# Kernel optimization log

Hardware: AMD Instinct MI355X
Metric: run time of the kernel (lower is better)

The kernel has to match this reference:

```python
import jax, jax.numpy as jnp
import numpy as np

N = 50000      # nodes
E = 800000     # edges (avg degree 16)
D_IN = 128
H = 128
D_OUT = 64
L = 3          # num GCNConv layers


def setup_inputs() -> dict:
    key = jax.random.key(0)
    ks = jax.random.split(key, 9)
    x = jax.random.normal(ks[0], (N, D_IN), jnp.float32)
    edge_index = jax.random.randint(ks[1], (2, E), 0, N, dtype=jnp.int32)
    s_in = 1.0 / np.sqrt(D_IN)
    s_h = 1.0 / np.sqrt(H)
    W1 = jax.random.normal(ks[2], (D_IN, H), jnp.float32) * s_in
    b1 = jnp.zeros((H,), jnp.float32)
    Wc = jax.random.normal(ks[3], (L, H, H), jnp.float32) * s_h
    bc = jnp.zeros((L, H), jnp.float32)
    W2 = jax.random.normal(ks[4], (H, D_OUT), jnp.float32) * s_h
    b2 = jnp.zeros((D_OUT,), jnp.float32)
    return {"x": x, "edge_index": edge_index, "W1": W1, "b1": b1,
            "Wc": Wc, "bc": bc, "W2": W2, "b2": b2}


def reference(x, edge_index, W1, b1, Wc, bc, W2, b2):
    n = x.shape[0]
    src, dst = edge_index[0], edge_index[1]
    # GCNConv normalization with self-loops: deg[i] = 1 + in-degree(i)
    deg = jnp.zeros((n,), x.dtype).at[dst].add(1.0) + 1.0
    dis = jax.lax.rsqrt(deg)                       # D^{-1/2}
    norm = dis[src] * dis[dst]                     # per-edge norm, [E]
    self_norm = (dis * dis)[:, None]               # self-loop norm, [n,1]
    # dnn1: Linear + ReLU
    h = jax.nn.relu(x @ W1 + b1)
    # GCNConv layers: x' = D^{-1/2}(A+I)D^{-1/2} X W + b
    for l in range(Wc.shape[0]):
        hw = h @ Wc[l]                             # [n, H]
        msg = hw[src] * norm[:, None]              # gather + scale, [E, H]
        agg = jax.ops.segment_sum(msg, dst, num_segments=n)
        h = agg + self_norm * hw + bc[l]
    # dnn2: Linear
    return h @ W2 + b2
```

## Files before the change

### kernel.cpp

```cpp
#include <hip/hip_runtime.h>
#include <hip/hip_fp16.h>


typedef _Float16 f16;
typedef __attribute__((ext_vector_type(8))) _Float16 f16x8;
typedef __attribute__((ext_vector_type(4))) float f32x4;

constexpr int H = 128;
constexpr int CH = 512;


__global__ __launch_bounds__(256) void k_degree(const int* __restrict__ dst,
                                                int* __restrict__ cnt,
                                                int* __restrict__ rank, int E) {
    int e = blockIdx.x * 256 + threadIdx.x;
    if (e < E) rank[e] = atomicAdd(&cnt[dst[e]], 1);
}

__global__ __launch_bounds__(CH) void k_scan1(const int* __restrict__ cnt,
                                              int* __restrict__ roff,
                                              int* __restrict__ csum,
                                              float* __restrict__ dis,
                                              float* __restrict__ dis2, int n) {
    __shared__ int sh[CH];
    int t = threadIdx.x;
    int i = blockIdx.x * CH + t;
    int v = (i < n) ? cnt[i] : 0;
    if (i < n) {
        float r = rsqrtf((float)(v + 1));
        dis[i] = r;
        dis2[i] = r * r;
    }
    sh[t] = v;
    __syncthreads();
    for (int off = 1; off < CH; off <<= 1) {
        int x = (t >= off) ? sh[t - off] : 0;
        __syncthreads();
        sh[t] += x;
        __syncthreads();
    }
    if (i < n) roff[i] = sh[t] - v;
    if (t == CH - 1) csum[blockIdx.x] = sh[t];
}

__global__ __launch_bounds__(256) void k_scan2(const int* __restrict__ csum,
                                               int* __restrict__ coff, int nch) {
    __shared__ int sh[256];
    int t = threadIdx.x;
    int v = (t < nch) ? csum[t] : 0;
    sh[t] = v;
    __syncthreads();
    for (int off = 1; off < 256; off <<= 1) {
        int x = (t >= off) ? sh[t - off] : 0;
        __syncthreads();
        sh[t] += x;
        __syncthreads();
    }
    if (t < nch) coff[t] = sh[t] - v;
}

__global__ __launch_bounds__(256) void k_scan3(int* __restrict__ roff,
                                               const int* __restrict__ coff,
                                               int n, int E) {
    int i = blockIdx.x * 256 + threadIdx.x;
    if (i < n) roff[i] += coff[i / CH];
    if (i == 0) roff[n] = E;
}

__global__ __launch_bounds__(256) void k_fill(const int* __restrict__ src,
                                              const int* __restrict__ dst,
                                              const int* __restrict__ rank,
                                              const int* __restrict__ roff,
                                              const float* __restrict__ dis,
                                              unsigned long long* __restrict__ edata,
                                              int E) {
    int e = blockIdx.x * 256 + threadIdx.x;
    if (e < E) {
        int d = dst[e], s = src[e];
        int pos = roff[d] + rank[e];
        float nm = dis[s] * dis[d];
        unsigned long long v = (unsigned long long)(unsigned)s |
                               ((unsigned long long)__float_as_uint(nm) << 32);
        atomicExch(&edata[pos], v);
    }
}


__global__ __launch_bounds__(256) void k_cvt_w(const float* __restrict__ W1,
                                               const float* __restrict__ Wc,
                                               const float* __restrict__ W2,
                                               f16* __restrict__ BT1,
                                               f16* __restrict__ BTc,
                                               f16* __restrict__ BT2) {
    int i = blockIdx.x * 256 + threadIdx.x;
    if (i < 16384) {
        int c = i >> 7, k = i & 127;
        BT1[i] = (f16)W1[k * 128 + c];
    } else if (i < 65536) {
        int j = i - 16384;
        int l = j >> 14, r = j & 16383;
        int c = r >> 7, k = r & 127;
        BTc[j] = (f16)Wc[l * 16384 + k * 128 + c];
    } else if (i < 73728) {
        int j = i - 65536;
        int c = j >> 7, k = j & 127;
        BT2[j] = (f16)W2[k * 64 + c];
    }
}


template <int NCOLS, int MODE, bool AF32>
__global__ __launch_bounds__(256) void k_gemm16(const void* __restrict__ Av,
                                                const f16* __restrict__ BT,
                                                const float* __restrict__ bias,
                                                void* __restrict__ Cv, int n) {
    constexpr int CT = NCOLS / 16;
    constexpr int BSTR = H + 8;
    __shared__ f16 Bs[NCOLS * BSTR];

    const int tid = threadIdx.x;
    constexpr int CHUNKS = NCOLS * H / (256 * 8);
#pragma unroll
    for (int it = 0; it < CHUNKS; ++it) {
        int idx = tid + it * 256;
        int r = idx >> 4;
        int c8 = idx & 15;
        *(f16x8*)&Bs[r * BSTR + c8 * 8] = *(const f16x8*)&BT[r * H + c8 * 8];
    }
    __syncthreads();

    const int l = tid & 63;
    const int w = tid >> 6;
    const int lrow = l & 15;
    const int lk = (l >> 4) * 8;
    int arow = blockIdx.x * 64 + w * 16 + lrow;
    int arc = arow < n ? arow : n - 1;

    f16x8 a[4];
    if constexpr (AF32) {
        const float* ap = (const float*)Av + (size_t)arc * H;
#pragma unroll
        for (int ks = 0; ks < 4; ++ks) {
            float4 u = *(const float4*)&ap[ks * 32 + lk];
            float4 v = *(const float4*)&ap[ks * 32 + lk + 4];
            f16x8 t;
            t[0] = (f16)u.x; t[1] = (f16)u.y; t[2] = (f16)u.z; t[3] = (f16)u.w;
            t[4] = (f16)v.x; t[5] = (f16)v.y; t[6] = (f16)v.z; t[7] = (f16)v.w;
            a[ks] = t;
        }
    } else {
        const f16* ap = (const f16*)Av + (size_t)arc * H;
#pragma unroll
        for (int ks = 0; ks < 4; ++ks) a[ks] = *(const f16x8*)&ap[ks * 32 + lk];
    }

    f32x4 acc[CT];
#pragma unroll
    for (int ct = 0; ct < CT; ++ct) acc[ct] = (f32x4)(0.f);

#pragma unroll
    for (int ks = 0; ks < 4; ++ks) {
#pragma unroll
        for (int ct = 0; ct < CT; ++ct) {
            f16x8 b = *(const f16x8*)&Bs[(ct * 16 + lrow) * BSTR + ks * 32 + lk];
            acc[ct] = __builtin_amdgcn_mfma_f32_16x16x32_f16(a[ks], b, acc[ct], 0, 0, 0);
        }
    }

    const int rbase = blockIdx.x * 64 + w * 16 + (l >> 4) * 4;
#pragma unroll
    for (int ct = 0; ct < CT; ++ct) {
        int col = ct * 16 + lrow;
        float bv = 0.f;
        if constexpr (MODE != 0) bv = bias[col];
#pragma unroll
        for (int r = 0; r < 4; ++r) {
            int row = rbase + r;
            if (row >= n) continue;
            float v = acc[ct][r] + bv;
            if constexpr (MODE == 1) v = fmaxf(v, 0.f);
            if constexpr (MODE == 2)
                ((float*)Cv)[(size_t)row * NCOLS + col] = v;
            else
                ((f16*)Cv)[(size_t)row * NCOLS + col] = (f16)v;
        }
    }
}


__global__ __launch_bounds__(256) void k_agg16(const __half2* __restrict__ hw,
                                               const int* __restrict__ roff,
                                               const long long* __restrict__ edata,
                                               const float* __restrict__ dis2,
                                               const float* __restrict__ bias,
                                               unsigned int* __restrict__ hout, int n) {
    int wave = threadIdx.x >> 6;
    int lane = threadIdx.x & 63;
    int node = blockIdx.x * 4 + wave;
    if (node >= n) return;

    int e0 = roff[node];
    int e1 = roff[node + 1];

    float2 sv = __half22float2(hw[(size_t)node * 64 + lane]);
    float d2 = dis2[node];
    float ax = sv.x * d2, ay = sv.y * d2;

    int e = e0;
    for (; e + 8 <= e1; e += 8) {
        long long ed[8];
#pragma unroll
        for (int j = 0; j < 8; ++j) ed[j] = __builtin_nontemporal_load(&edata[e + j]);
        float2 v[8];
#pragma unroll
        for (int j = 0; j < 8; ++j)
            v[j] = __half22float2(hw[(size_t)(unsigned)(ed[j] & 0xffffffff) * 64 + lane]);
#pragma unroll
        for (int j = 0; j < 8; ++j) {
            float nm = __int_as_float((int)(ed[j] >> 32));
            ax = fmaf(nm, v[j].x, ax);
            ay = fmaf(nm, v[j].y, ay);
        }
    }
    for (; e + 2 <= e1; e += 2) {
        long long d0 = __builtin_nontemporal_load(&edata[e]);
        long long d1 = __builtin_nontemporal_load(&edata[e + 1]);
        float2 v0 = __half22float2(hw[(size_t)(unsigned)(d0 & 0xffffffff) * 64 + lane]);
        float2 v1 = __half22float2(hw[(size_t)(unsigned)(d1 & 0xffffffff) * 64 + lane]);
        ax = fmaf(__int_as_float((int)(d0 >> 32)), v0.x, ax);
        ay = fmaf(__int_as_float((int)(d0 >> 32)), v0.y, ay);
        ax = fmaf(__int_as_float((int)(d1 >> 32)), v1.x, ax);
        ay = fmaf(__int_as_float((int)(d1 >> 32)), v1.y, ay);
    }
    for (; e < e1; ++e) {
        long long d0 = __builtin_nontemporal_load(&edata[e]);
        float2 v0 = __half22float2(hw[(size_t)(unsigned)(d0 & 0xffffffff) * 64 + lane]);
        float nm = __int_as_float((int)(d0 >> 32));
        ax = fmaf(nm, v0.x, ax);
        ay = fmaf(nm, v0.y, ay);
    }

    float2 b = ((const float2*)bias)[lane];
    ax += b.x; ay += b.y;
    __half2 r = __float22half2_rn(make_float2(ax, ay));
    __builtin_nontemporal_store(*(unsigned int*)&r, &hout[(size_t)node * 64 + lane]);
}


extern "C" void kernel_launch(void* const* d_in, const int* in_sizes, int n_in,
                              void* d_out, int out_size, void* d_ws, size_t ws_size,
                              hipStream_t stream) {
    const float* x  = (const float*)d_in[0];
    const int*   ei = (const int*)d_in[1];
    const float* W1 = (const float*)d_in[2];
    const float* b1 = (const float*)d_in[3];
    const float* Wc = (const float*)d_in[4];
    const float* bc = (const float*)d_in[5];
    const float* W2 = (const float*)d_in[6];
    const float* b2 = (const float*)d_in[7];
    float* out = (float*)d_out;

    const int n = in_sizes[0] / H;
    const int E = in_sizes[1] / 2;
    const int* src = ei;
    const int* dst = ei + E;

    char* p = (char*)d_ws;
    auto alloc = [&](size_t b) -> void* {
        void* r = (void*)p;
        p += (b + 255) & ~(size_t)255;
        return r;
    };
    f16*   h    = (f16*)alloc((size_t)n * H * 2);
    f16*   hw   = (f16*)alloc((size_t)n * H * 2);
    f16*   BT1  = (f16*)alloc(16384 * 2);
    f16*   BTc  = (f16*)alloc(3 * 16384 * 2);
    f16*   BT2  = (f16*)alloc(8192 * 2);
    int*   cnt  = (int*)alloc((size_t)n * 4);
    int*   rank = (int*)alloc((size_t)E * 4);
    int*   roff = (int*)alloc((size_t)(n + 1) * 4);
    const int nch = (n + CH - 1) / CH;
    int*   csum = (int*)alloc((size_t)nch * 4);
    int*   coff = (int*)alloc((size_t)nch * 4);
    unsigned long long* edata = (unsigned long long*)alloc((size_t)E * 8);
    float* dis  = (float*)alloc((size_t)n * 4);
    float* dis2 = (float*)alloc((size_t)n * 4);

    hipMemsetAsync(cnt, 0, (size_t)n * 4, stream);

    k_degree<<<(E + 255) / 256, 256, 0, stream>>>(dst, cnt, rank, E);
    k_scan1<<<nch, CH, 0, stream>>>(cnt, roff, csum, dis, dis2, n);
    k_scan2<<<1, 256, 0, stream>>>(csum, coff, nch);
    k_scan3<<<(n + 255) / 256, 256, 0, stream>>>(roff, coff, n, E);
    k_fill<<<(E + 255) / 256, 256, 0, stream>>>(src, dst, rank, roff, dis, edata, E);

    k_cvt_w<<<288, 256, 0, stream>>>(W1, Wc, W2, BT1, BTc, BT2);

    const int gblk = (n + 63) / 64;
    k_gemm16<128, 1, true><<<gblk, 256, 0, stream>>>(x, BT1, b1, h, n);
    for (int l = 0; l < 3; ++l) {
        k_gemm16<128, 0, false><<<gblk, 256, 0, stream>>>(h, BTc + (size_t)l * 16384, nullptr, hw, n);
        k_agg16<<<(n + 3) / 4, 256, 0, stream>>>((const __half2*)hw, roff, (const long long*)edata,
                                                 dis2, bc + (size_t)l * H, (unsigned int*)h, n);
    }
    k_gemm16<64, 2, false><<<gblk, 256, 0, stream>>>(h, BT2, b2, out, n);
}
```

Before: 337.6 us.

## Pad CSR rows to multiples of eight and software-pipeline edge loads in aggregation

The CSR layout now pads each node's edge list to a multiple of 8 and zero-fills the padding, so the aggregation kernel can run a single unrolled 8-wide loop with no remainder loops. Each iteration prefetches the next 8 edge records before gathering the current ones. The kernel also moves to 512-thread blocks with normal rather than nontemporal loads and stores, and the weight conversion is merged into the degree kernel to save a launch. In exchange it adds a memset of the enlarged edge buffer and wasted gathers on padded zero-weight entries, which all read node 0.

```diff
diff --git a/kernel.cpp b/kernel.cpp
--- a/kernel.cpp
+++ b/kernel.cpp
@@ -10,11 +10,34 @@
 constexpr int CH = 512;
 
 
-__global__ __launch_bounds__(256) void k_degree(const int* __restrict__ dst,
-                                                int* __restrict__ cnt,
-                                                int* __restrict__ rank, int E) {
-    int e = blockIdx.x * 256 + threadIdx.x;
-    if (e < E) rank[e] = atomicAdd(&cnt[dst[e]], 1);
+__global__ __launch_bounds__(256) void k_degree_cvtw(const int* __restrict__ dst,
+                                                     int* __restrict__ cnt,
+                                                     int* __restrict__ rank, int E, int EB,
+                                                     const float* __restrict__ W1,
+                                                     const float* __restrict__ Wc,
+                                                     const float* __restrict__ W2,
+                                                     f16* __restrict__ BT1,
+                                                     f16* __restrict__ BTc,
+                                                     f16* __restrict__ BT2) {
+    if (blockIdx.x < (unsigned)EB) {
+        int e = blockIdx.x * 256 + threadIdx.x;
+        if (e < E) rank[e] = atomicAdd(&cnt[dst[e]], 1);
+    } else {
+        int i = (blockIdx.x - EB) * 256 + threadIdx.x;
+        if (i < 16384) {
+            int c = i >> 7, k = i & 127;
+            BT1[i] = (f16)W1[k * 128 + c];
+        } else if (i < 65536) {
+            int j = i - 16384;
+            int l = j >> 14, r = j & 16383;
+            int c = r >> 7, k = r & 127;
+            BTc[j] = (f16)Wc[l * 16384 + k * 128 + c];
+        } else if (i < 73728) {
+            int j = i - 65536;
+            int c = j >> 7, k = j & 127;
+            BT2[j] = (f16)W2[k * 64 + c];
+        }
+    }
 }
 
 __global__ __launch_bounds__(CH) void k_scan1(const int* __restrict__ cnt,
@@ -31,7 +54,8 @@
         dis[i] = r;
         dis2[i] = r * r;
     }
-    sh[t] = v;
+    int pd = (v + 7) & ~7;
+    sh[t] = pd;
     __syncthreads();
     for (int off = 1; off < CH; off <<= 1) {
         int x = (t >= off) ? sh[t - off] : 0;
@@ -39,12 +63,13 @@
         sh[t] += x;
         __syncthreads();
     }
-    if (i < n) roff[i] = sh[t] - v;
+    if (i < n) roff[i] = sh[t] - pd;
     if (t == CH - 1) csum[blockIdx.x] = sh[t];
 }
 
 __global__ __launch_bounds__(256) void k_scan2(const int* __restrict__ csum,
-                                               int* __restrict__ coff, int nch) {
+                                               int* __restrict__ coff,
+                                               int* __restrict__ roff, int n, int nch) {
     __shared__ int sh[256];
     int t = threadIdx.x;
     int v = (t < nch) ? csum[t] : 0;
@@ -57,14 +82,13 @@
         __syncthreads();
     }
     if (t < nch) coff[t] = sh[t] - v;
+    if (t == nch - 1) roff[n] = sh[t];
 }
 
 __global__ __launch_bounds__(256) void k_scan3(int* __restrict__ roff,
-                                               const int* __restrict__ coff,
-                                               int n, int E) {
+                                               const int* __restrict__ coff, int n) {
     int i = blockIdx.x * 256 + threadIdx.x;
     if (i < n) roff[i] += coff[i / CH];
-    if (i == 0) roff[n] = E;
 }
 
 __global__ __launch_bounds__(256) void k_fill(const int* __restrict__ src,
@@ -86,29 +110,6 @@
 }
 
 
-__global__ __launch_bounds__(256) void k_cvt_w(const float* __restrict__ W1,
-                                               const float* __restrict__ Wc,
-                                               const float* __restrict__ W2,
-                                               f16* __restrict__ BT1,
-                                               f16* __restrict__ BTc,
-                                               f16* __restrict__ BT2) {
-    int i = blockIdx.x * 256 + threadIdx.x;
-    if (i < 16384) {
-        int c = i >> 7, k = i & 127;
-        BT1[i] = (f16)W1[k * 128 + c];
-    } else if (i < 65536) {
-        int j = i - 16384;
-        int l = j >> 14, r = j & 16383;
-        int c = r >> 7, k = r & 127;
-        BTc[j] = (f16)Wc[l * 16384 + k * 128 + c];
-    } else if (i < 73728) {
-        int j = i - 65536;
-        int c = j >> 7, k = j & 127;
-        BT2[j] = (f16)W2[k * 64 + c];
-    }
-}
-
-
 template <int NCOLS, int MODE, bool AF32>
 __global__ __launch_bounds__(256) void k_gemm16(const void* __restrict__ Av,
                                                 const f16* __restrict__ BT,
@@ -188,7 +189,7 @@
 }
 
 
-__global__ __launch_bounds__(256) void k_agg16(const __half2* __restrict__ hw,
+__global__ __launch_bounds__(512) void k_agg16(const __half2* __restrict__ hw,
                                                const int* __restrict__ roff,
                                                const long long* __restrict__ edata,
                                                const float* __restrict__ dis2,
@@ -196,54 +197,46 @@
                                                unsigned int* __restrict__ hout, int n) {
     int wave = threadIdx.x >> 6;
     int lane = threadIdx.x & 63;
-    int node = blockIdx.x * 4 + wave;
+    int node = blockIdx.x * 8 + wave;
     if (node >= n) return;
 
-    int e0 = roff[node];
-    int e1 = roff[node + 1];
+    int e = roff[node];
+    const int e1 = roff[node + 1];
 
     float2 sv = __half22float2(hw[(size_t)node * 64 + lane]);
     float d2 = dis2[node];
     float ax = sv.x * d2, ay = sv.y * d2;
 
-    int e = e0;
-    for (; e + 8 <= e1; e += 8) {
-        long long ed[8];
-#pragma unroll
-        for (int j = 0; j < 8; ++j) ed[j] = __builtin_nontemporal_load(&edata[e + j]);
+    long long cur[8], nxt[8];
+    if (e < e1) {
+#pragma unroll
+        for (int j = 0; j < 8; ++j) cur[j] = edata[e + j];
+    }
+    while (e < e1) {
+        int en = e + 8;
+        if (en < e1) {
+#pragma unroll
+            for (int j = 0; j < 8; ++j) nxt[j] = edata[en + j];
+        }
         float2 v[8];
 #pragma unroll
         for (int j = 0; j < 8; ++j)
-            v[j] = __half22float2(hw[(size_t)(unsigned)(ed[j] & 0xffffffff) * 64 + lane]);
+            v[j] = __half22float2(hw[(size_t)(unsigned)(cur[j] & 0xffffffff) * 64 + lane]);
 #pragma unroll
         for (int j = 0; j < 8; ++j) {
-            float nm = __int_as_float((int)(ed[j] >> 32));
+            float nm = __int_as_float((int)(cur[j] >> 32));
             ax = fmaf(nm, v[j].x, ax);
             ay = fmaf(nm, v[j].y, ay);
         }
-    }
-    for (; e + 2 <= e1; e += 2) {
-        long long d0 = __builtin_nontemporal_load(&edata[e]);
-        long long d1 = __builtin_nontemporal_load(&edata[e + 1]);
-        float2 v0 = __half22float2(hw[(size_t)(unsigned)(d0 & 0xffffffff) * 64 + lane]);
-        float2 v1 = __half22float2(hw[(size_t)(unsigned)(d1 & 0xffffffff) * 64 + lane]);
-        ax = fmaf(__int_as_float((int)(d0 >> 32)), v0.x, ax);
-        ay = fmaf(__int_as_float((int)(d0 >> 32)), v0.y, ay);
-        ax = fmaf(__int_as_float((int)(d1 >> 32)), v1.x, ax);
-        ay = fmaf(__int_as_float((int)(d1 >> 32)), v1.y, ay);
-    }
-    for (; e < e1; ++e) {
-        long long d0 = __builtin_nontemporal_load(&edata[e]);
-        float2 v0 = __half22float2(hw[(size_t)(unsigned)(d0 & 0xffffffff) * 64 + lane]);
-        float nm = __int_as_float((int)(d0 >> 32));
-        ax = fmaf(nm, v0.x, ax);
-        ay = fmaf(nm, v0.y, ay);
+#pragma unroll
+        for (int j = 0; j < 8; ++j) cur[j] = nxt[j];
+        e = en;
     }
 
     float2 b = ((const float2*)bias)[lane];
     ax += b.x; ay += b.y;
     __half2 r = __float22half2_rn(make_float2(ax, ay));
-    __builtin_nontemporal_store(*(unsigned int*)&r, &hout[(size_t)node * 64 + lane]);
+    hout[(size_t)node * 64 + lane] = *(unsigned int*)&r;
 }
 
 
@@ -282,25 +275,27 @@
     const int nch = (n + CH - 1) / CH;
     int*   csum = (int*)alloc((size_t)nch * 4);
     int*   coff = (int*)alloc((size_t)nch * 4);
-    unsigned long long* edata = (unsigned long long*)alloc((size_t)E * 8);
+    const size_t ecap = (size_t)E + 8 * (size_t)n;
+    unsigned long long* edata = (unsigned long long*)alloc(ecap * 8);
     float* dis  = (float*)alloc((size_t)n * 4);
     float* dis2 = (float*)alloc((size_t)n * 4);
 
     hipMemsetAsync(cnt, 0, (size_t)n * 4, stream);
-
-    k_degree<<<(E + 255) / 256, 256, 0, stream>>>(dst, cnt, rank, E);
+    hipMemsetAsync(edata, 0, ecap * 8, stream);
+
+    const int EB = (E + 255) / 256;
+    k_degree_cvtw<<<EB + 288, 256, 0, stream>>>(dst, cnt, rank, E, EB,
+                                                W1, Wc, W2, BT1, BTc, BT2);
     k_scan1<<<nch, CH, 0, stream>>>(cnt, roff, csum, dis, dis2, n);
-    k_scan2<<<1, 256, 0, stream>>>(csum, coff, nch);
-    k_scan3<<<(n + 255) / 256, 256, 0, stream>>>(roff, coff, n, E);
-    k_fill<<<(E + 255) / 256, 256, 0, stream>>>(src, dst, rank, roff, dis, edata, E);
-
-    k_cvt_w<<<288, 256, 0, stream>>>(W1, Wc, W2, BT1, BTc, BT2);
+    k_scan2<<<1, 256, 0, stream>>>(csum, coff, roff, n, nch);
+    k_scan3<<<(n + 255) / 256, 256, 0, stream>>>(roff, coff, n);
+    k_fill<<<EB, 256, 0, stream>>>(src, dst, rank, roff, dis, edata, E);
 
     const int gblk = (n + 63) / 64;
     k_gemm16<128, 1, true><<<gblk, 256, 0, stream>>>(x, BT1, b1, h, n);
     for (int l = 0; l < 3; ++l) {
         k_gemm16<128, 0, false><<<gblk, 256, 0, stream>>>(h, BTc + (size_t)l * 16384, nullptr, hw, n);
-        k_agg16<<<(n + 3) / 4, 256, 0, stream>>>((const __half2*)hw, roff, (const long long*)edata,
+        k_agg16<<<(n + 7) / 8, 512, 0, stream>>>((const __half2*)hw, roff, (const long long*)edata,
                                                  dis2, bc + (size_t)l * H, (unsigned int*)h, n);
     }
     k_gemm16<64, 2, false><<<gblk, 256, 0, stream>>>(h, BT2, b2, out, n);
```

After: 319.1 us. 5.5% less time.
